# Kernel tuning notes

Measured on AMD Instinct MI355X. Metric: run time of the kernel, lower is better.

## Reference

```python
import jax, jax.numpy as jnp
import numpy as np

EPS = 1e-5  # BatchNorm eps (torch default)
PAD = 1
K = 9  # 3x3 kernel points

def conv3x3(x, w, b):
    # x: [B,C,H,W], w: [O,C,3,3]
    y = jax.lax.conv_general_dilated(x, w, (1, 1), ((PAD, PAD), (PAD, PAD)),
                                     dimension_numbers=('NCHW', 'OIHW', 'NCHW'))
    return y + b[None, :, None, None]

def deform_conv2d(x, offset, mask, weight, bias):
    # Modulated deformable conv v2, stride 1, pad 1, 3x3 kernel.
    # x: [B,C,H,W]; offset: [B,2K,H,W] (first K = dy, last K = dx); mask: [B,K,H,W]
    B, C, H, W = x.shape
    ki, kj = jnp.meshgrid(jnp.arange(3), jnp.arange(3), indexing='ij')
    ki = ki.reshape(K).astype(x.dtype)
    kj = kj.reshape(K).astype(x.dtype)
    dy = offset[:, :K].transpose(0, 2, 3, 1)   # [B,H,W,K]
    dx = offset[:, K:].transpose(0, 2, 3, 1)
    m = mask.transpose(0, 2, 3, 1)             # [B,H,W,K]
    hs = jnp.arange(H, dtype=x.dtype)
    ws = jnp.arange(W, dtype=x.dtype)
    py = hs[None, :, None, None] - PAD + ki[None, None, None, :] + dy  # [B,H,W,K]
    px = ws[None, None, :, None] - PAD + kj[None, None, None, :] + dx
    y0 = jnp.floor(py)
    x0 = jnp.floor(px)
    wy1 = py - y0
    wx1 = px - x0
    wy0 = 1.0 - wy1
    wx0 = 1.0 - wx1

    def gather(yi, xi):
        valid = ((yi >= 0) & (yi < H) & (xi >= 0) & (xi < W)).astype(x.dtype)
        yc = jnp.clip(yi, 0, H - 1).astype(jnp.int32)
        xc = jnp.clip(xi, 0, W - 1).astype(jnp.int32)
        g = jax.vmap(lambda img, yb, xb: img[:, yb, xb])(x, yc, xc)  # [B,C,H,W,K]
        return g * valid[:, None]

    val = (gather(y0, x0) * (wy0 * wx0)[:, None]
           + gather(y0, x0 + 1.0) * (wy0 * wx1)[:, None]
           + gather(y0 + 1.0, x0) * (wy1 * wx0)[:, None]
           + gather(y0 + 1.0, x0 + 1.0) * (wy1 * wx1)[:, None])
    val = val * m[:, None]  # modulation
    out = jnp.einsum('bchwk,ock->bohw', val, weight.reshape(weight.shape[0], C, K))
    return out + bias[None, :, None, None]

def dcnv2(x, w_om, b_om, w, b, gamma, beta, mean, var):
    om = conv3x3(x, w_om, b_om)               # [B,27,H,W]
    o1, o2, mr = jnp.split(om, 3, axis=1)
    offset = jnp.concatenate([o1, o2], axis=1)  # [B,18,H,W]
    mask = jax.nn.sigmoid(mr)
    y = deform_conv2d(x, offset, mask, w, b)
    scale = (gamma / jnp.sqrt(var + EPS))[None, :, None, None]
    y = (y - mean[None, :, None, None]) * scale + beta[None, :, None, None]
    return jax.nn.silu(y)

def setup_inputs() -> dict:
    key = jax.random.key(0)
    ks = jax.random.split(key, 9)
    B, C, H, W = 4, 256, 128, 128
    C4 = C // 4
    return {
        'x': jax.random.normal(ks[0], (B, C, H, W), jnp.float32),
        'w': jax.random.normal(ks[1], (4, C4, C4, 3, 3), jnp.float32) * 0.05,
        'b': jax.random.normal(ks[2], (4, C4), jnp.float32) * 0.05,
        'w_om': jax.random.normal(ks[3], (4, 27, C4, 3, 3), jnp.float32) * 0.01,
        'b_om': jax.random.normal(ks[4], (4, 27), jnp.float32) * 0.01,
        'gamma': jax.random.normal(ks[5], (4, C4), jnp.float32) * 0.1 + 1.0,
        'beta': jax.random.normal(ks[6], (4, C4), jnp.float32) * 0.1,
        'mean': jax.random.normal(ks[7], (4, C4), jnp.float32) * 0.1,
        'var': jax.random.uniform(ks[8], (4, C4), jnp.float32, minval=0.5, maxval=1.5),
    }

def reference(x, w, b, w_om, b_om, gamma, beta, mean, var):
    B, C, H, W = x.shape
    C4 = C // 4
    # channel-split into 4 independent groups, vmap identical DCNv2 over groups
    xg = x.reshape(B, 4, C4, H, W).transpose(1, 0, 2, 3, 4)  # [4,B,C4,H,W]
    yg = jax.vmap(dcnv2)(xg, w_om, b_om, w, b, gamma, beta, mean, var)
    return yg.transpose(1, 0, 2, 3, 4).reshape(B, C, H, W)
```

## Files before the change

### kernel.cpp

```cpp
#include <hip/hip_runtime.h>
#include <math.h>

#define Hs 128
#define Ws 128
#define HWs 16384

typedef __attribute__((ext_vector_type(8))) short short8;
typedef __attribute__((ext_vector_type(8))) __bf16 bf16x8;
typedef __attribute__((ext_vector_type(4))) float f32x4;
typedef __attribute__((ext_vector_type(2))) float f32x2;

static __device__ __forceinline__ float bf2f(unsigned short u) {
    union { unsigned int i; float f; } v; v.i = ((unsigned int)u) << 16; return v.f;
}
static __device__ __forceinline__ unsigned short f2bf(float f) {
    unsigned int u = __builtin_bit_cast(unsigned int, f);
    return (unsigned short)((u + 0x7fffu + ((u >> 16) & 1u)) >> 16);
}
static __device__ __forceinline__ f32x4 mfma16(short8 a, short8 b, f32x4 c) {
    return __builtin_amdgcn_mfma_f32_16x16x32_bf16(
        __builtin_bit_cast(bf16x8, a), __builtin_bit_cast(bf16x8, b), c, 0, 0, 0);
}
static __device__ __forceinline__ f32x2 pk_mul(f32x2 a, f32x2 b) {
    f32x2 d;
    asm("v_pk_mul_f32 %0, %1, %2" : "=v"(d) : "v"(a), "v"(b));
    return d;
}
static __device__ __forceinline__ f32x2 pk_fma(f32x2 a, f32x2 b, f32x2 c) {
    f32x2 d;
    asm("v_pk_fma_f32 %0, %1, %2, %3" : "=v"(d) : "v"(a), "v"(b), "v"(c));
    return d;
}
static __device__ __forceinline__ unsigned int cvt_pk_bf16(float lo, float hi) {
    unsigned int d;
    asm("v_cvt_pk_bf16_f32 %0, %1, %2" : "=v"(d) : "v"(lo), "v"(hi));
    return d;
}
static __device__ __forceinline__ f32x2 bfpair(unsigned int u) {
    union { unsigned int i[2]; f32x2 f; } v;
    v.i[0] = u << 16;
    v.i[1] = u & 0xffff0000u;
    return v.f;
}
static __device__ __forceinline__ void xcd_map(int f, int& img, int& tile) {
    img  = ((f & 7) << 1) | ((f >> 3) & 1);
    tile = f >> 4;
}

__global__ __launch_bounds__(256) void k_xt(const float* __restrict__ x,
                                            const float* __restrict__ w,
                                            const float* __restrict__ b,
                                            const float* __restrict__ w_om,
                                            const float* __restrict__ gamma,
                                            const float* __restrict__ beta,
                                            const float* __restrict__ mean,
                                            const float* __restrict__ var,
                                            unsigned short* __restrict__ xT,
                                            unsigned short* __restrict__ w2,
                                            unsigned short* __restrict__ wom2,
                                            float* __restrict__ scsh) {
    const int tid = threadIdx.x;
    const int f = blockIdx.y * 256 + blockIdx.x;
    if (f < 576) {
        int idx = f * 256 + tid;
        if (idx < 4 * 64 * 576) {
            int go = idx / 576;
            int ck = idx - go * 576;
            int k = ck >> 6, c = ck & 63;
            w2[idx] = f2bf(w[go * 576 + c * 9 + k]);
        }
        if (idx < 4 * 32 * 576) {
            int gj = idx / 576;
            int g = gj >> 5, j = gj & 31;
            int ck = idx - gj * 576;
            int k = ck >> 6, c = ck & 63;
            float v = (j < 27) ? w_om[(g * 27 + j) * 576 + c * 9 + k] : 0.f;
            wom2[idx] = f2bf(v);
        }
        if (idx < 256) {
            float sc = gamma[idx] * rsqrtf(var[idx] + 1e-5f);
            scsh[idx] = sc;
            scsh[256 + idx] = (b[idx] - mean[idx]) * sc + beta[idx];
        }
    }

    int img, tile;
    xcd_map(f, img, tile);
    const int g = img >> 2, bb = img & 3;
    const int p0 = tile * 64;
    __shared__ float t[64 * 65];

    const float* xg = x + (size_t)(bb * 256 + g * 64) * HWs + p0;
    const int l16 = tid & 15, grp = tid >> 4;
#pragma unroll
    for (int pass = 0; pass < 4; ++pass) {
        int c = pass * 16 + grp;
        float4 v = *(const float4*)(xg + (size_t)c * HWs + l16 * 4);
        float* tr = &t[c * 65 + l16 * 4];
        tr[0] = v.x; tr[1] = v.y; tr[2] = v.z; tr[3] = v.w;
    }
    __syncthreads();
    const int p = tid >> 2, c16 = (tid & 3) * 16;
    unsigned short* dst = xT + (size_t)img * HWs * 64 + (size_t)(p0 + p) * 64 + c16;
    unsigned int rr[8];
#pragma unroll
    for (int q = 0; q < 8; ++q)
        rr[q] = cvt_pk_bf16(t[(c16 + 2 * q) * 65 + p], t[(c16 + 2 * q + 1) * 65 + p]);
    *(uint4*)dst       = make_uint4(rr[0], rr[1], rr[2], rr[3]);
    *(uint4*)(dst + 8) = make_uint4(rr[4], rr[5], rr[6], rr[7]);
}

__global__ __launch_bounds__(256, 3) void k_off(const unsigned short* __restrict__ xT,
                                                const unsigned short* __restrict__ wom2,
                                                const float* __restrict__ b_om,
                                                float* __restrict__ om) {
    const int f = blockIdx.y * 128 + blockIdx.x;
    int img, h;
    xcd_map(f, img, h);
    const int g = img >> 2;
    const int tid = threadIdx.x;
    const int lane = tid & 63, wv = tid >> 6;
    const int mt = wv & 1, nh = wv >> 1;
    const int m = lane & 15, q = lane >> 4;

    __shared__ unsigned short xrow[3 * 130 * 64];

    const unsigned short* xTi = xT + (size_t)img * HWs * 64;
    for (int i = tid; i < 3 * 130 * 8; i += 256) {
        int rr = i / 1040;
        int rem = i - rr * 1040;
        int px = rem >> 3, j = rem & 7;
        int gh = h + rr - 1, gw = px - 1;
        uint4 v = make_uint4(0, 0, 0, 0);
        if (gh >= 0 && gh < Hs && gw >= 0 && gw < Ws)
            v = *(const uint4*)(xTi + (size_t)(gh * Ws + gw) * 64 + j * 8);
        *(uint4*)&xrow[(rr * 130 + px) * 64 + (j ^ (px & 7)) * 8] = v;
    }

    short8 afrag[18];
    const unsigned short* wb = wom2 + (size_t)(g * 32 + mt * 16 + m) * 576 + q * 8;
#pragma unroll
    for (int t = 0; t < 18; ++t) afrag[t] = *(const short8*)(wb + t * 32);

    f32x4 acc[4];
#pragma unroll
    for (int t = 0; t < 4; ++t) acc[t] = (f32x4){0.f, 0.f, 0.f, 0.f};

    __syncthreads();

#pragma unroll
    for (int k = 0; k < 9; ++k) {
        const int ki = k / 3, kj = k - ki * 3;
#pragma unroll
        for (int s = 0; s < 2; ++s) {
#pragma unroll
            for (int t = 0; t < 4; ++t) {
                int px = (nh * 4 + t) * 16 + m + kj;
                int gran = (s * 4 + q) ^ (px & 7);
                short8 bfrag = *(const short8*)&xrow[(ki * 130 + px) * 64 + gran * 8];
                acc[t] = mfma16(afrag[k * 2 + s], bfrag, acc[t]);
            }
        }
    }

    float* omi = om + (size_t)img * 27 * HWs + h * Ws;
#pragma unroll
    for (int t = 0; t < 4; ++t) {
#pragma unroll
        for (int r = 0; r < 4; ++r) {
            int j = mt * 16 + q * 4 + r;
            if (j < 27) {
                float v = acc[t][r] + b_om[g * 27 + j];
                if (j >= 18) v = 1.f / (1.f + __expf(-v));
                omi[(size_t)j * HWs + (nh * 4 + t) * 16 + m] = v;
            }
        }
    }
}

__global__ __launch_bounds__(256, 4) void k_def(const unsigned short* __restrict__ xT,
                                                const float* __restrict__ om,
                                                const unsigned short* __restrict__ w2,
                                                const float* __restrict__ scsh,
                                                float* __restrict__ out) {
    const int f = blockIdx.y * 256 + blockIdx.x;
    int img, tile;
    xcd_map(f, img, tile);
    const int g = img >> 2, bb = img & 3;
    const int p0 = tile * 64;
    const int tid = threadIdx.x;
    const int lane = tid & 63, wv = tid >> 6;
    const int m = lane & 15, q = lane >> 4;

    __shared__ int   pO[4][576];
    __shared__ float pW[4][576];
    __shared__ unsigned short val[2][64 * 64];
    __shared__ float lsc[64], lsh[64];

    if (tid < 64) {
        lsc[tid] = scsh[g * 64 + tid];
        lsh[tid] = scsh[256 + g * 64 + tid];
    }

    const float* omg = om + (size_t)img * 27 * HWs;
    for (int idx = tid; idx < 576; idx += 256) {
        int k = idx >> 6, pp = idx & 63;
        int p = p0 + pp;
        int h = p >> 7, w = p & 127;
        float dy = omg[k * HWs + p];
        float dx = omg[(9 + k) * HWs + p];
        float mk = omg[(18 + k) * HWs + p];
        int ki = k / 3, kj = k - ki * 3;
        float py = (float)(h - 1 + ki) + dy;
        float px = (float)(w - 1 + kj) + dx;
        float fy = floorf(py), fx = floorf(px);
        float wy1 = py - fy, wx1 = px - fx;
        float wy0 = 1.f - wy1, wx0 = 1.f - wx1;
        int y0 = (int)fy, x0 = (int)fx, y1 = y0 + 1, x1 = x0 + 1;
        bool vy0 = (y0 >= 0) && (y0 < Hs), vy1 = (y1 >= 0) && (y1 < Hs);
        bool vx0 = (x0 >= 0) && (x0 < Ws), vx1 = (x1 >= 0) && (x1 < Ws);
        int cy0 = min(max(y0, 0), Hs - 1), cy1 = min(max(y1, 0), Hs - 1);
        int cx0 = min(max(x0, 0), Ws - 1), cx1 = min(max(x1, 0), Ws - 1);
        pO[0][idx] = cy0 * Ws + cx0;
        pO[1][idx] = cy0 * Ws + cx1;
        pO[2][idx] = cy1 * Ws + cx0;
        pO[3][idx] = cy1 * Ws + cx1;
        pW[0][idx] = (vy0 && vx0) ? wy0 * wx0 * mk : 0.f;
        pW[1][idx] = (vy0 && vx1) ? wy0 * wx1 * mk : 0.f;
        pW[2][idx] = (vy1 && vx0) ? wy1 * wx0 * mk : 0.f;
        pW[3][idx] = (vy1 && vx1) ? wy1 * wx1 * mk : 0.f;
    }

    short8 afrag[18];
    const unsigned short* wb = w2 + (size_t)(g * 64 + wv * 16 + m) * 576 + q * 8;
#pragma unroll
    for (int t = 0; t < 18; ++t) afrag[t] = *(const short8*)(wb + t * 32);

    f32x4 acc[4];
#pragma unroll
    for (int t = 0; t < 4; ++t) acc[t] = (f32x4){0.f, 0.f, 0.f, 0.f};

    const unsigned short* xTi = xT + (size_t)img * HWs * 64;
    const int p = tid >> 2, c4 = tid & 3;
    const int wr_sw = ((p >> 1) & 7) << 3;
    const int rd_sw = ((m >> 1) & 7) << 3;

    __syncthreads();

    uint4 gth[2][8];
    float wfb[2][4];
    auto fetch = [&](int k, int bf) {
        const int kb = k * 64 + p;
        const int off0 = pO[0][kb], off1 = pO[1][kb], off2 = pO[2][kb], off3 = pO[3][kb];
        wfb[bf][0] = pW[0][kb]; wfb[bf][1] = pW[1][kb];
        wfb[bf][2] = pW[2][kb]; wfb[bf][3] = pW[3][kb];
        const unsigned short* s0 = xTi + (size_t)off0 * 64 + c4 * 16;
        const unsigned short* s1 = xTi + (size_t)off1 * 64 + c4 * 16;
        const unsigned short* s2 = xTi + (size_t)off2 * 64 + c4 * 16;
        const unsigned short* s3 = xTi + (size_t)off3 * 64 + c4 * 16;
        gth[bf][0] = *(const uint4*)(s0);
        gth[bf][1] = *(const uint4*)(s1);
        gth[bf][2] = *(const uint4*)(s2);
        gth[bf][3] = *(const uint4*)(s3);
        gth[bf][4] = *(const uint4*)(s0 + 8);
        gth[bf][5] = *(const uint4*)(s1 + 8);
        gth[bf][6] = *(const uint4*)(s2 + 8);
        gth[bf][7] = *(const uint4*)(s3 + 8);
    };
    fetch(0, 0);

#pragma unroll
    for (int k = 0; k < 9; ++k) {
        const int cb = k & 1, nb = cb ^ 1;
        if (k < 8) fetch(k + 1, nb);
        unsigned short* vb = &val[cb][0];
        const float* wf = wfb[cb];
        f32x2 w0p = {wf[0], wf[0]}, w1p = {wf[1], wf[1]};
        f32x2 w2p = {wf[2], wf[2]}, w3p = {wf[3], wf[3]};
#pragma unroll
        for (int it = 0; it < 2; ++it) {
            const int oc8 = (2 * c4 + it) * 8;
            unsigned int rr[4];
#pragma unroll
            for (int e = 0; e < 4; ++e) {
                f32x2 x0 = bfpair(((const unsigned int*)&gth[cb][it * 4 + 0])[e]);
                f32x2 x1 = bfpair(((const unsigned int*)&gth[cb][it * 4 + 1])[e]);
                f32x2 x2 = bfpair(((const unsigned int*)&gth[cb][it * 4 + 2])[e]);
                f32x2 x3 = bfpair(((const unsigned int*)&gth[cb][it * 4 + 3])[e]);
                f32x2 a = pk_mul(x0, w0p);
                a = pk_fma(x1, w1p, a);
                a = pk_fma(x2, w2p, a);
                a = pk_fma(x3, w3p, a);
                rr[e] = cvt_pk_bf16(a[0], a[1]);
            }
            *(uint4*)&vb[p * 64 + (oc8 ^ wr_sw)] = make_uint4(rr[0], rr[1], rr[2], rr[3]);
        }
        __syncthreads();
        const unsigned short* vr = &val[cb][0];
#pragma unroll
        for (int s = 0; s < 2; ++s) {
#pragma unroll
            for (int t = 0; t < 4; ++t) {
                const int row = t * 16 + m;
                short8 bfrag = *(const short8*)&vr[row * 64 + ((s * 32 + q * 8) ^ rd_sw)];
                acc[t] = mfma16(afrag[k * 2 + s], bfrag, acc[t]);
            }
        }
    }

    float* outg = out + ((size_t)bb * 256 + g * 64) * HWs + p0;
#pragma unroll
    for (int t = 0; t < 4; ++t) {
#pragma unroll
        for (int r = 0; r < 4; ++r) {
            int o = wv * 16 + q * 4 + r;
            float y = acc[t][r] * lsc[o] + lsh[o];
            outg[(size_t)o * HWs + t * 16 + m] = y / (1.f + __expf(-y));
        }
    }
}

extern "C" void kernel_launch(void* const* d_in, const int* in_sizes, int n_in,
                              void* d_out, int out_size, void* d_ws, size_t ws_size,
                              hipStream_t stream) {
    const float* x     = (const float*)d_in[0];
    const float* w     = (const float*)d_in[1];
    const float* b     = (const float*)d_in[2];
    const float* w_om  = (const float*)d_in[3];
    const float* b_om  = (const float*)d_in[4];
    const float* gamma = (const float*)d_in[5];
    const float* beta  = (const float*)d_in[6];
    const float* mean  = (const float*)d_in[7];
    const float* var   = (const float*)d_in[8];
    float* out = (float*)d_out;

    char* ws = (char*)d_ws;
    float* om            = (float*)ws;
    unsigned short* xT   = (unsigned short*)(ws + 28311552);
    unsigned short* w2   = (unsigned short*)(ws + 61865984);
    unsigned short* wom2 = (unsigned short*)(ws + 62160896);
    float* scsh          = (float*)(ws + 62308352);

    hipLaunchKernelGGL(k_xt, dim3(256, 16), dim3(256), 0, stream,
                       x, w, b, w_om, gamma, beta, mean, var, xT, w2, wom2, scsh);
    hipLaunchKernelGGL(k_off, dim3(128, 16), dim3(256), 0, stream, xT, wom2, b_om, om);
    hipLaunchKernelGGL(k_def, dim3(256, 16), dim3(256), 0, stream, xT, om, w2, scsh, out);
}
```

Measured before the change: 271.8 us.

## Drop XCD block remap, stream weight fragments per tap, lower k_def min occupancy

Removes the XCD-aware block index remapping in all three kernels and uses plain blockIdx.x/y for tile and image. In k_def, the 18 preloaded weight fragments are no longer held in registers for the whole loop. Instead, two fragments per kernel tap are double-buffered alongside the gather prefetch, which cuts register pressure. At the same time the launch bound's minimum blocks per SM goes from 4 to 2, giving the compiler more register headroom, possibly at the cost of occupancy and of L2 locality across XCDs.

```diff
diff --git a/kernel.cpp b/kernel.cpp
--- a/kernel.cpp
+++ b/kernel.cpp
@@ -41,10 +41,6 @@
     v.i[0] = u << 16;
     v.i[1] = u & 0xffff0000u;
     return v.f;
-}
-static __device__ __forceinline__ void xcd_map(int f, int& img, int& tile) {
-    img  = ((f & 7) << 1) | ((f >> 3) & 1);
-    tile = f >> 4;
 }
 
 __global__ __launch_bounds__(256) void k_xt(const float* __restrict__ x,
@@ -84,10 +80,9 @@
         }
     }
 
-    int img, tile;
-    xcd_map(f, img, tile);
+    const int img = blockIdx.y;
     const int g = img >> 2, bb = img & 3;
-    const int p0 = tile * 64;
+    const int p0 = blockIdx.x * 64;
     __shared__ float t[64 * 65];
 
     const float* xg = x + (size_t)(bb * 256 + g * 64) * HWs + p0;
@@ -114,10 +109,9 @@
                                                 const unsigned short* __restrict__ wom2,
                                                 const float* __restrict__ b_om,
                                                 float* __restrict__ om) {
-    const int f = blockIdx.y * 128 + blockIdx.x;
-    int img, h;
-    xcd_map(f, img, h);
+    const int img = blockIdx.y;
     const int g = img >> 2;
+    const int h = blockIdx.x;
     const int tid = threadIdx.x;
     const int lane = tid & 63, wv = tid >> 6;
     const int mt = wv & 1, nh = wv >> 1;
@@ -178,16 +172,14 @@
     }
 }
 
-__global__ __launch_bounds__(256, 4) void k_def(const unsigned short* __restrict__ xT,
+__global__ __launch_bounds__(256, 2) void k_def(const unsigned short* __restrict__ xT,
                                                 const float* __restrict__ om,
                                                 const unsigned short* __restrict__ w2,
                                                 const float* __restrict__ scsh,
                                                 float* __restrict__ out) {
-    const int f = blockIdx.y * 256 + blockIdx.x;
-    int img, tile;
-    xcd_map(f, img, tile);
+    const int img = blockIdx.y;
     const int g = img >> 2, bb = img & 3;
-    const int p0 = tile * 64;
+    const int p0 = blockIdx.x * 64;
     const int tid = threadIdx.x;
     const int lane = tid & 63, wv = tid >> 6;
     const int m = lane & 15, q = lane >> 4;
@@ -231,11 +223,6 @@
         pW[3][idx] = (vy1 && vx1) ? wy1 * wx1 * mk : 0.f;
     }
 
-    short8 afrag[18];
-    const unsigned short* wb = w2 + (size_t)(g * 64 + wv * 16 + m) * 576 + q * 8;
-#pragma unroll
-    for (int t = 0; t < 18; ++t) afrag[t] = *(const short8*)(wb + t * 32);
-
     f32x4 acc[4];
 #pragma unroll
     for (int t = 0; t < 4; ++t) acc[t] = (f32x4){0.f, 0.f, 0.f, 0.f};
@@ -246,6 +233,13 @@
     const int rd_sw = ((m >> 1) & 7) << 3;
 
     __syncthreads();
+
+    short8 af[2][2];
+    const unsigned short* wb = w2 + (size_t)(g * 64 + wv * 16 + m) * 576 + q * 8;
+    auto fetchA = [&](int k, int bf) {
+        af[bf][0] = *(const short8*)(wb + (k * 2 + 0) * 32);
+        af[bf][1] = *(const short8*)(wb + (k * 2 + 1) * 32);
+    };
 
     uint4 gth[2][8];
     float wfb[2][4];
@@ -268,11 +262,15 @@
         gth[bf][7] = *(const uint4*)(s3 + 8);
     };
     fetch(0, 0);
+    fetchA(0, 0);
 
 #pragma unroll
     for (int k = 0; k < 9; ++k) {
         const int cb = k & 1, nb = cb ^ 1;
-        if (k < 8) fetch(k + 1, nb);
+        if (k < 8) {
+            fetch(k + 1, nb);
+            fetchA(k + 1, nb);
+        }
         unsigned short* vb = &val[cb][0];
         const float* wf = wfb[cb];
         f32x2 w0p = {wf[0], wf[0]}, w1p = {wf[1], wf[1]};
@@ -303,7 +301,7 @@
             for (int t = 0; t < 4; ++t) {
                 const int row = t * 16 + m;
                 short8 bfrag = *(const short8*)&vr[row * 64 + ((s * 32 + q * 8) ^ rd_sw)];
-                acc[t] = mfma16(afrag[k * 2 + s], bfrag, acc[t]);
+                acc[t] = mfma16(af[cb][s], bfrag, acc[t]);
             }
         }
     }
```

Measured after the change: 243.0 us. 1.12x faster.
